# Kernel optimization log

Measured on AMD Instinct MI355X. Metric: run time of the kernel, lower is better.

## Reference

```python
import jax, jax.numpy as jnp
import numpy as np

EPS = 1e-6


def setup_inputs() -> dict:
    key = jax.random.key(0)
    k1, k2, k3 = jax.random.split(key, 3)
    B, S, H, I = 4, 2048, 2048, 8192
    x = jax.random.normal(k1, (B, S, H), dtype=jnp.float32)
    scale = jnp.ones((H,), dtype=jnp.float32)
    ln_bias = jnp.zeros((H,), dtype=jnp.float32)
    # kernel_1: [hidden, num_activations=2, intermediate] (GeGLU)
    kernel_1 = jax.random.normal(k2, (H, 2, I), dtype=jnp.float32) * (1.0 / np.sqrt(H))
    # kernel_2: [intermediate, hidden]
    kernel_2 = jax.random.normal(k3, (I, H), dtype=jnp.float32) * (1.0 / np.sqrt(I))
    return {"x": x, "scale": scale, "ln_bias": ln_bias, "kernel_1": kernel_1, "kernel_2": kernel_2}


def reference(x, scale, ln_bias, kernel_1, kernel_2):
    # LayerNorm over last axis (zero_centered_gamma=False)
    mu = jnp.mean(x, axis=-1, keepdims=True)
    var = jnp.mean(jnp.square(x - mu), axis=-1, keepdims=True)
    y = (x - mu) * jax.lax.rsqrt(var + EPS) * scale + ln_bias
    # First GEMM: [B,S,H] x [H, act=2, I] -> [B,S,2,I]
    h = jnp.einsum("bsh,hai->bsai", y, kernel_1)
    # Gated activation: gelu(branch 0) * linear(branch 1)  (flax gelu: approximate tanh)
    z = jax.nn.gelu(h[..., 0, :], approximate=True) * h[..., 1, :]
    # Dropout rate = 0 (deterministic) -> no-op
    # Second GEMM: [B,S,I] x [I,H] -> [B,S,H]
    out = jnp.einsum("bsi,ih->bsh", z, kernel_2)
    return out
```

## Files before the change

### kernel.cpp

```cpp
#include <hip/hip_runtime.h>
#include <hip/hip_bf16.h>
#include <stdint.h>

typedef __attribute__((ext_vector_type(8))) __bf16 bf16x8;
typedef __attribute__((ext_vector_type(4))) float f32x4;

static constexpr int kTokens = 8192;
static constexpr int kHid    = 2048;
static constexpr int kInter  = 8192;
static constexpr int kN1     = 16384;

__device__ __forceinline__ void async16(const void* g, void* l) {
  using gp = const __attribute__((address_space(1))) unsigned int*;
  using lp = __attribute__((address_space(3))) unsigned int*;
  __builtin_amdgcn_global_load_lds((gp)(uintptr_t)g,
                                   (lp)(unsigned int)(uintptr_t)l, 16, 0, 0);
}

__global__ __launch_bounds__(256) void ln_kernel(
    const float* __restrict__ x, const float* __restrict__ gamma,
    const float* __restrict__ beta, __hip_bfloat16* __restrict__ y) {
  const int t = threadIdx.x;
  const size_t row = blockIdx.x;
  const float* xr = x + row * kHid;
  float4 v0 = ((const float4*)xr)[2 * t];
  float4 v1 = ((const float4*)xr)[2 * t + 1];
  float s  = v0.x + v0.y + v0.z + v0.w + v1.x + v1.y + v1.z + v1.w;
  float s2 = v0.x*v0.x + v0.y*v0.y + v0.z*v0.z + v0.w*v0.w
           + v1.x*v1.x + v1.y*v1.y + v1.z*v1.z + v1.w*v1.w;
#pragma unroll
  for (int off = 1; off < 64; off <<= 1) {
    s  += __shfl_xor(s, off, 64);
    s2 += __shfl_xor(s2, off, 64);
  }
  __shared__ float red[8];
  const int w = t >> 6;
  if ((t & 63) == 0) { red[w] = s; red[4 + w] = s2; }
  __syncthreads();
  s  = red[0] + red[1] + red[2] + red[3];
  s2 = red[4] + red[5] + red[6] + red[7];
  const float mu = s * (1.0f / kHid);
  const float rs = rsqrtf(s2 * (1.0f / kHid) - mu * mu + 1e-6f);
  float4 g0 = ((const float4*)gamma)[2 * t], g1 = ((const float4*)gamma)[2 * t + 1];
  float4 b0 = ((const float4*)beta)[2 * t],  b1 = ((const float4*)beta)[2 * t + 1];
  union { __hip_bfloat16 h[8]; uint4 u; } pk;
  pk.h[0] = __float2bfloat16((v0.x - mu) * rs * g0.x + b0.x);
  pk.h[1] = __float2bfloat16((v0.y - mu) * rs * g0.y + b0.y);
  pk.h[2] = __float2bfloat16((v0.z - mu) * rs * g0.z + b0.z);
  pk.h[3] = __float2bfloat16((v0.w - mu) * rs * g0.w + b0.w);
  pk.h[4] = __float2bfloat16((v1.x - mu) * rs * g1.x + b1.x);
  pk.h[5] = __float2bfloat16((v1.y - mu) * rs * g1.y + b1.y);
  pk.h[6] = __float2bfloat16((v1.z - mu) * rs * g1.z + b1.z);
  pk.h[7] = __float2bfloat16((v1.w - mu) * rs * g1.w + b1.w);
  ((uint4*)(y + row * kHid))[t] = pk.u;
}

template <bool INTERLEAVE>
__global__ __launch_bounds__(256) void cvt_tr(
    const float* __restrict__ src, __hip_bfloat16* __restrict__ dst,
    int K, int N) {
  __shared__ float tile[64][65];
  const int nb = blockIdx.x * 64;
  const int kb = blockIdx.y * 64;
  const int t = threadIdx.x;
#pragma unroll
  for (int it = 0; it < 16; ++it) {
    int p = t + it * 256;
    int lk = p >> 6, ln = p & 63;
    int n = nb + ln;
    int col = INTERLEAVE ? ((((n >> 4) & 1) << 13) + (((n >> 5) << 4) | (n & 15)))
                         : n;
    tile[lk][ln] = src[(size_t)(kb + lk) * N + col];
  }
  __syncthreads();
#pragma unroll
  for (int it = 0; it < 16; ++it) {
    int p = t + it * 256;
    int ln = p >> 6, lk = p & 63;
    dst[(size_t)(nb + ln) * K + kb + lk] = __float2bfloat16(tile[lk][ln]);
  }
}

#define SLOT_A(b, h) ((b) * 65536 + (h) * 16384)
#define SLOT_B(b, h) ((b) * 65536 + 32768 + (h) * 16384)
#define SLOT_DUMMY 131072

template <int EPI, int NXTLOG>
__global__ __launch_bounds__(512, 2) void gemm8p(
    const __hip_bfloat16* __restrict__ A, const __hip_bfloat16* __restrict__ B,
    void* __restrict__ Cout, int M, int N, int K) {
  __shared__ __align__(16) char smem[139264];
  char* const sm = (char*)smem;

  const int t = threadIdx.x;
  const int lane = t & 63;
  const int wave = t >> 6;
  const int wm = wave >> 2;
  const int wn = wave & 3;

  const int nwg = (int)gridDim.x;
  const int wg = ((int)blockIdx.x & 7) * (nwg >> 3) + ((int)blockIdx.x >> 3);
  const int bx = wg & ((1 << NXTLOG) - 1);
  const int by = wg >> NXTLOG;
  const size_t m0 = (size_t)by * 256;
  const size_t n0 = (size_t)bx * 256;

  const int srow = t >> 3;
  const int scsrc = (t & 7) ^ (srow & 7);
  const __hip_bfloat16* const gA = A + (m0 + srow) * K + scsrc * 8;
  const __hip_bfloat16* const gB = B + (n0 + srow) * K + scsrc * 8;
  const size_t K64  = (size_t)64 * K;
  const size_t K128 = (size_t)128 * K;
  const int t16 = t * 16;
  char* const dm = sm + SLOT_DUMMY + t16;

  const int col = lane & 15, q = lane >> 4;
  const int cs0 = (q ^ (col & 7)) * 16;
  const int cs1 = ((4 + q) ^ (col & 7)) * 16;
  const int aO0 = wm * 16384 + col * 128 + cs0;
  const int aO1 = wm * 16384 + col * 128 + cs1;
  const int bO0 = 32768 + (wn >> 1) * 16384 + ((wn & 1) * 64 + col) * 128 + cs0;
  const int bO1 = 32768 + (wn >> 1) * 16384 + ((wn & 1) * 64 + col) * 128 + cs1;

  f32x4 acc[8][4] = {};
  bf16x8 af[4][2], bf[4][2];

  const int NT = K >> 6;
  const int L  = NT >> 1;

#define STG_A(tile, h, buf)                                           \
  do {                                                                \
    const __hip_bfloat16* _s = gA + (size_t)(tile) * 64 + (h) * K128; \
    char* _d = sm + SLOT_A(buf, h) + t16;                             \
    async16(_s, _d);                                                  \
    async16(_s + K64, _d + 8192);                                     \
  } while (0)
#define STG_B(tile, h, buf)                                           \
  do {                                                                \
    const __hip_bfloat16* _s = gB + (size_t)(tile) * 64 + (h) * K128; \
    char* _d = sm + SLOT_B(buf, h) + t16;                             \
    async16(_s, _d);                                                  \
    async16(_s + K64, _d + 8192);                                     \
  } while (0)
#define STG_A_G(tile, h, buf)                  \
  do {                                         \
    if ((tile) < NT) { STG_A(tile, h, buf); }  \
    else { async16(A, dm); async16(A, dm); }   \
  } while (0)
#define STG_B_G(tile, h, buf)                  \
  do {                                         \
    if ((tile) < NT) { STG_B(tile, h, buf); }  \
    else { async16(A, dm); async16(A, dm); }   \
  } while (0)

#define LOAD_A(buf, mh)                                                        \
  { _Pragma("unroll") for (int ii = 0; ii < 4; ++ii) {                         \
      af[ii][0] = *(const bf16x8*)(sm + (buf)*65536 + aO0 + (mh)*8192 + ii*2048); \
      af[ii][1] = *(const bf16x8*)(sm + (buf)*65536 + aO1 + (mh)*8192 + ii*2048); \
  } }
#define LOAD_B(buf, nh)                                                        \
  { _Pragma("unroll") for (int jj = 0; jj < 2; ++jj) {                         \
      bf[(nh)*2 + jj][0] = *(const bf16x8*)(sm + (buf)*65536 + bO0 + ((nh)*2 + jj)*2048); \
      bf[(nh)*2 + jj][1] = *(const bf16x8*)(sm + (buf)*65536 + bO1 + ((nh)*2 + jj)*2048); \
  } }

#define MFMA_QUAD(mh, nh)                                                     \
  { _Pragma("unroll") for (int kk = 0; kk < 2; ++kk)                          \
    _Pragma("unroll") for (int ii = 0; ii < 4; ++ii)                          \
    _Pragma("unroll") for (int jj = 0; jj < 2; ++jj)                          \
      acc[(mh)*4 + ii][(nh)*2 + jj] = __builtin_amdgcn_mfma_f32_16x16x32_bf16( \
          af[ii][kk], bf[(nh)*2 + jj][kk], acc[(mh)*4 + ii][(nh)*2 + jj], 0, 0, 0); }

#define PHASE_MID()                                  \
  __builtin_amdgcn_s_barrier();                      \
  asm volatile("s_waitcnt lgkmcnt(0)" ::: "memory"); \
  __builtin_amdgcn_s_setprio(1)
#define PHASE_MID_VM()                               \
  asm volatile("s_waitcnt vmcnt(4)" ::: "memory");   \
  __builtin_amdgcn_s_barrier();                      \
  asm volatile("s_waitcnt lgkmcnt(0)" ::: "memory"); \
  __builtin_amdgcn_s_setprio(1)
#define PHASE_END()                                  \
  __builtin_amdgcn_s_setprio(0);                     \
  __builtin_amdgcn_s_barrier()

  STG_A(0, 0, 0);
  STG_A(0, 1, 0);
  STG_B(0, 0, 0);
  STG_B(0, 1, 0);
  STG_B(1, 0, 1);
  STG_B(1, 1, 1);
  asm volatile("s_waitcnt vmcnt(4)" ::: "memory");
  __builtin_amdgcn_s_barrier();

#pragma unroll 1
  for (int i = 0; i < L; ++i) {
    const int t1 = 2 * i + 1, t2 = 2 * i + 2, t3 = 2 * i + 3;
    LOAD_A(0, 0) LOAD_B(0, 0)
    STG_A(t1, 0, 1);
    PHASE_MID(); MFMA_QUAD(0, 0) PHASE_END();
    LOAD_B(0, 1)
    STG_A(t1, 1, 1);
    PHASE_MID(); MFMA_QUAD(0, 1) PHASE_END();
    LOAD_A(0, 1)
    STG_B_G(t2, 0, 0);
    PHASE_MID(); MFMA_QUAD(1, 0) PHASE_END();
    STG_B_G(t2, 1, 0);
    PHASE_MID_VM(); MFMA_QUAD(1, 1) PHASE_END();
    LOAD_A(1, 0) LOAD_B(1, 0)
    STG_A_G(t2, 0, 0);
    PHASE_MID(); MFMA_QUAD(0, 0) PHASE_END();
    LOAD_B(1, 1)
    STG_A_G(t2, 1, 0);
    PHASE_MID(); MFMA_QUAD(0, 1) PHASE_END();
    LOAD_A(1, 1)
    STG_B_G(t3, 0, 1);
    PHASE_MID(); MFMA_QUAD(1, 0) PHASE_END();
    STG_B_G(t3, 1, 1);
    PHASE_MID_VM(); MFMA_QUAD(1, 1) PHASE_END();
  }
  asm volatile("s_waitcnt vmcnt(0)" ::: "memory");

  const int gr0 = (int)m0 + wm * 128 + q * 4;
  if (EPI == 0) {
    float* Cf = (float*)Cout;
    const int gc0 = (int)n0 + wn * 64 + col;
#pragma unroll
    for (int mi = 0; mi < 8; ++mi)
#pragma unroll
      for (int j = 0; j < 4; ++j) {
        size_t base = (size_t)(gr0 + mi * 16) * N + gc0 + j * 16;
#pragma unroll
        for (int r = 0; r < 4; ++r) Cf[base + (size_t)r * N] = acc[mi][j][r];
      }
  } else {
    __hip_bfloat16* Z = (__hip_bfloat16*)Cout;
    const int ldz = N >> 1;
    const size_t ib0 = (n0 >> 1) + wn * 32 + col;
#pragma unroll
    for (int mi = 0; mi < 8; ++mi)
#pragma unroll
      for (int tp = 0; tp < 2; ++tp) {
        const f32x4 gg = acc[mi][2 * tp];
        const f32x4 ll = acc[mi][2 * tp + 1];
        size_t base = (size_t)(gr0 + mi * 16) * ldz + ib0 + tp * 16;
#pragma unroll
        for (int r = 0; r < 4; ++r) {
          float xv = gg[r];
          float u = 0.7978845608028654f * xv * (1.0f + 0.044715f * xv * xv);
          float sg = __builtin_amdgcn_rcpf(1.0f + __expf(-2.0f * u));
          Z[base + (size_t)r * ldz] = __float2bfloat16(xv * sg * ll[r]);
        }
      }
  }
}

extern "C" void kernel_launch(void* const* d_in, const int* in_sizes, int n_in,
                              void* d_out, int out_size, void* d_ws, size_t ws_size,
                              hipStream_t stream) {
  const float* x     = (const float*)d_in[0];
  const float* gamma = (const float*)d_in[1];
  const float* beta  = (const float*)d_in[2];
  const float* W1    = (const float*)d_in[3];
  const float* W2    = (const float*)d_in[4];
  float* out = (float*)d_out;

  char* ws = (char*)d_ws;
  __hip_bfloat16* yb  = (__hip_bfloat16*)ws;
  __hip_bfloat16* w1t = (__hip_bfloat16*)(ws + (32ull << 20));
  __hip_bfloat16* w2t = (__hip_bfloat16*)(ws + (96ull << 20));
  __hip_bfloat16* z   = (__hip_bfloat16*)(ws + (128ull << 20));
  (void)in_sizes; (void)n_in; (void)out_size; (void)ws_size;

  ln_kernel<<<kTokens, 256, 0, stream>>>(x, gamma, beta, yb);
  cvt_tr<true ><<<dim3(kN1 / 64, kHid / 64), 256, 0, stream>>>(W1, w1t, kHid, kN1);
  cvt_tr<false><<<dim3(kHid / 64, kInter / 64), 256, 0, stream>>>(W2, w2t, kInter, kHid);
  gemm8p<1, 6><<<dim3((kN1 / 256) * (kTokens / 256)), 512, 0, stream>>>(
      yb, w1t, (void*)z, kTokens, kN1, kHid);
  gemm8p<0, 3><<<dim3((kHid / 256) * (kTokens / 256)), 512, 0, stream>>>(
      z, w2t, (void*)out, kTokens, kHid, kInter);
}
```

Before: 1.003 ms.

## Restructure GEMM prefetch to full-tile double buffering and M-major tile order

The GEMM main loop now stages whole A and B k-tiles (four async loads each) into the alternate buffer two phases ahead, instead of staggering half-tile A loads inside the current iteration. The prologue preloads both buffers, and the wait counts change to vmcnt(8) plus an lgkmcnt(8) wait before the first phase. Workgroup-to-tile mapping also changes from N-fastest to M-fastest (32 M tiles per column), which alters L2 reuse of the weight panels. The deeper prefetch keeps more loads in flight per wave, and the new tile order may reduce reuse of the activation rows.

```diff
diff --git a/kernel.cpp b/kernel.cpp
--- a/kernel.cpp
+++ b/kernel.cpp
@@ -85,7 +85,7 @@
 #define SLOT_B(b, h) ((b) * 65536 + 32768 + (h) * 16384)
 #define SLOT_DUMMY 131072
 
-template <int EPI, int NXTLOG>
+template <int EPI>
 __global__ __launch_bounds__(512, 2) void gemm8p(
     const __hip_bfloat16* __restrict__ A, const __hip_bfloat16* __restrict__ B,
     void* __restrict__ Cout, int M, int N, int K) {
@@ -100,8 +100,8 @@
 
   const int nwg = (int)gridDim.x;
   const int wg = ((int)blockIdx.x & 7) * (nwg >> 3) + ((int)blockIdx.x >> 3);
-  const int bx = wg & ((1 << NXTLOG) - 1);
-  const int by = wg >> NXTLOG;
+  const int by = wg & 31;
+  const int bx = wg >> 5;
   const size_t m0 = (size_t)by * 256;
   const size_t n0 = (size_t)bx * 256;
 
@@ -128,29 +128,35 @@
   const int NT = K >> 6;
   const int L  = NT >> 1;
 
-#define STG_A(tile, h, buf)                                           \
-  do {                                                                \
-    const __hip_bfloat16* _s = gA + (size_t)(tile) * 64 + (h) * K128; \
-    char* _d = sm + SLOT_A(buf, h) + t16;                             \
-    async16(_s, _d);                                                  \
-    async16(_s + K64, _d + 8192);                                     \
-  } while (0)
-#define STG_B(tile, h, buf)                                           \
-  do {                                                                \
-    const __hip_bfloat16* _s = gB + (size_t)(tile) * 64 + (h) * K128; \
-    char* _d = sm + SLOT_B(buf, h) + t16;                             \
-    async16(_s, _d);                                                  \
-    async16(_s + K64, _d + 8192);                                     \
-  } while (0)
-#define STG_A_G(tile, h, buf)                  \
-  do {                                         \
-    if ((tile) < NT) { STG_A(tile, h, buf); }  \
-    else { async16(A, dm); async16(A, dm); }   \
-  } while (0)
-#define STG_B_G(tile, h, buf)                  \
-  do {                                         \
-    if ((tile) < NT) { STG_B(tile, h, buf); }  \
-    else { async16(A, dm); async16(A, dm); }   \
+#define STG_A2(tile, buf)                                \
+  do {                                                   \
+    const __hip_bfloat16* _s = gA + (size_t)(tile) * 64; \
+    char* _d = sm + SLOT_A(buf, 0) + t16;                \
+    async16(_s, _d);                                     \
+    async16(_s + K64, _d + 8192);                        \
+    async16(_s + K128, _d + 16384);                      \
+    async16(_s + K128 + K64, _d + 16384 + 8192);         \
+  } while (0)
+#define STG_B2(tile, buf)                                \
+  do {                                                   \
+    const __hip_bfloat16* _s = gB + (size_t)(tile) * 64; \
+    char* _d = sm + SLOT_B(buf, 0) + t16;                \
+    async16(_s, _d);                                     \
+    async16(_s + K64, _d + 8192);                        \
+    async16(_s + K128, _d + 16384);                      \
+    async16(_s + K128 + K64, _d + 16384 + 8192);         \
+  } while (0)
+#define STG_A2_G(tile, buf)                              \
+  do {                                                   \
+    if ((tile) < NT) { STG_A2(tile, buf); }              \
+    else { async16(A, dm); async16(A, dm);               \
+           async16(A, dm); async16(A, dm); }             \
+  } while (0)
+#define STG_B2_G(tile, buf)                              \
+  do {                                                   \
+    if ((tile) < NT) { STG_B2(tile, buf); }              \
+    else { async16(A, dm); async16(A, dm);               \
+           async16(A, dm); async16(A, dm); }             \
   } while (0)
 
 #define LOAD_A(buf, mh)                                                        \
@@ -175,8 +181,13 @@
   __builtin_amdgcn_s_barrier();                      \
   asm volatile("s_waitcnt lgkmcnt(0)" ::: "memory"); \
   __builtin_amdgcn_s_setprio(1)
+#define PHASE_MID12()                                \
+  asm volatile("s_waitcnt lgkmcnt(8)" ::: "memory"); \
+  __builtin_amdgcn_s_barrier();                      \
+  asm volatile("s_waitcnt lgkmcnt(0)" ::: "memory"); \
+  __builtin_amdgcn_s_setprio(1)
 #define PHASE_MID_VM()                               \
-  asm volatile("s_waitcnt vmcnt(4)" ::: "memory");   \
+  asm volatile("s_waitcnt vmcnt(8)" ::: "memory");   \
   __builtin_amdgcn_s_barrier();                      \
   asm volatile("s_waitcnt lgkmcnt(0)" ::: "memory"); \
   __builtin_amdgcn_s_setprio(1)
@@ -184,39 +195,33 @@
   __builtin_amdgcn_s_setprio(0);                     \
   __builtin_amdgcn_s_barrier()
 
-  STG_A(0, 0, 0);
-  STG_A(0, 1, 0);
-  STG_B(0, 0, 0);
-  STG_B(0, 1, 0);
-  STG_B(1, 0, 1);
-  STG_B(1, 1, 1);
-  asm volatile("s_waitcnt vmcnt(4)" ::: "memory");
+  STG_B2(0, 0);
+  STG_A2(0, 0);
+  STG_B2(1, 1);
+  STG_A2(1, 1);
+  asm volatile("s_waitcnt vmcnt(8)" ::: "memory");
   __builtin_amdgcn_s_barrier();
 
 #pragma unroll 1
   for (int i = 0; i < L; ++i) {
-    const int t1 = 2 * i + 1, t2 = 2 * i + 2, t3 = 2 * i + 3;
+    const int t2 = 2 * i + 2, t3 = 2 * i + 3;
     LOAD_A(0, 0) LOAD_B(0, 0)
-    STG_A(t1, 0, 1);
-    PHASE_MID(); MFMA_QUAD(0, 0) PHASE_END();
+    PHASE_MID12(); MFMA_QUAD(0, 0) PHASE_END();
     LOAD_B(0, 1)
-    STG_A(t1, 1, 1);
     PHASE_MID(); MFMA_QUAD(0, 1) PHASE_END();
     LOAD_A(0, 1)
-    STG_B_G(t2, 0, 0);
+    STG_B2_G(t2, 0);
     PHASE_MID(); MFMA_QUAD(1, 0) PHASE_END();
-    STG_B_G(t2, 1, 0);
+    STG_A2_G(t2, 0);
     PHASE_MID_VM(); MFMA_QUAD(1, 1) PHASE_END();
     LOAD_A(1, 0) LOAD_B(1, 0)
-    STG_A_G(t2, 0, 0);
-    PHASE_MID(); MFMA_QUAD(0, 0) PHASE_END();
+    PHASE_MID12(); MFMA_QUAD(0, 0) PHASE_END();
     LOAD_B(1, 1)
-    STG_A_G(t2, 1, 0);
     PHASE_MID(); MFMA_QUAD(0, 1) PHASE_END();
     LOAD_A(1, 1)
-    STG_B_G(t3, 0, 1);
+    STG_B2_G(t3, 1);
     PHASE_MID(); MFMA_QUAD(1, 0) PHASE_END();
-    STG_B_G(t3, 1, 1);
+    STG_A2_G(t3, 1);
     PHASE_MID_VM(); MFMA_QUAD(1, 1) PHASE_END();
   }
   asm volatile("s_waitcnt vmcnt(0)" ::: "memory");
@@ -275,8 +280,8 @@
   ln_kernel<<<kTokens, 256, 0, stream>>>(x, gamma, beta, yb);
   cvt_tr<true ><<<dim3(kN1 / 64, kHid / 64), 256, 0, stream>>>(W1, w1t, kHid, kN1);
   cvt_tr<false><<<dim3(kHid / 64, kInter / 64), 256, 0, stream>>>(W2, w2t, kInter, kHid);
-  gemm8p<1, 6><<<dim3((kN1 / 256) * (kTokens / 256)), 512, 0, stream>>>(
+  gemm8p<1><<<dim3((kN1 / 256) * (kTokens / 256)), 512, 0, stream>>>(
       yb, w1t, (void*)z, kTokens, kN1, kHid);
-  gemm8p<0, 3><<<dim3((kHid / 256) * (kTokens / 256)), 512, 0, stream>>>(
+  gemm8p<0><<<dim3((kHid / 256) * (kTokens / 256)), 512, 0, stream>>>(
       z, w2t, (void*)out, kTokens, kHid, kInter);
 }
```

Result: slower. 1.053 ms (+5.0%).

## Switch GEMM inner loop to 32x32x16 MFMA with 32-wide gate interleave

Applied to the files above, without the earlier changes.

Replaces the 16x16x32 bf16 MFMA tiling with 32x32x16 MFMA tiles, so each wave holds 4x2 32x32 accumulators. The LDS fragment reads and address precomputation are reworked to fit, and the W1 interleave granularity changes from 16 to 32 columns so gate and linear halves land in matching accumulator tiles. The epilogues are rewritten for the 32x32 output layout. The aim is fewer LDS reads per MFMA and higher MFMA throughput, at the cost of different register pressure and LDS bank-conflict behaviour.

```diff
diff --git a/kernel.cpp b/kernel.cpp
--- a/kernel.cpp
+++ b/kernel.cpp
@@ -4,6 +4,7 @@
 
 typedef __attribute__((ext_vector_type(8))) __bf16 bf16x8;
 typedef __attribute__((ext_vector_type(4))) float f32x4;
+typedef __attribute__((ext_vector_type(16))) float f32x16;
 
 static constexpr int kTokens = 8192;
 static constexpr int kHid    = 2048;
@@ -68,7 +69,7 @@
     int p = t + it * 256;
     int lk = p >> 6, ln = p & 63;
     int n = nb + ln;
-    int col = INTERLEAVE ? ((((n >> 4) & 1) << 13) + (((n >> 5) << 4) | (n & 15)))
+    int col = INTERLEAVE ? ((((n >> 5) & 1) << 13) + (((n >> 6) << 5) | (n & 31)))
                          : n;
     tile[lk][ln] = src[(size_t)(kb + lk) * N + col];
   }
@@ -114,16 +115,20 @@
   const int t16 = t * 16;
   char* const dm = sm + SLOT_DUMMY + t16;
 
-  const int col = lane & 15, q = lane >> 4;
-  const int cs0 = (q ^ (col & 7)) * 16;
-  const int cs1 = ((4 + q) ^ (col & 7)) * 16;
-  const int aO0 = wm * 16384 + col * 128 + cs0;
-  const int aO1 = wm * 16384 + col * 128 + cs1;
-  const int bO0 = 32768 + (wn >> 1) * 16384 + ((wn & 1) * 64 + col) * 128 + cs0;
-  const int bO1 = 32768 + (wn >> 1) * 16384 + ((wn & 1) * 64 + col) * 128 + cs1;
-
-  f32x4 acc[8][4] = {};
-  bf16x8 af[4][2], bf[4][2];
+  const int l31 = lane & 31, hi = lane >> 5, l7 = lane & 7;
+  int aAdr[2][4], bAdr[2][4];
+#pragma unroll
+  for (int b2 = 0; b2 < 2; ++b2)
+#pragma unroll
+    for (int ks = 0; ks < 4; ++ks) {
+      const int ch = (((ks << 1) | hi) ^ l7) << 4;
+      aAdr[b2][ks] = b2 * 65536 + (((wm << 7) + l31) << 7) + ch;
+      bAdr[b2][ks] = b2 * 65536 + 32768 + (((wn << 6) + l31) << 7) + ch;
+    }
+
+  f32x16 acc[4][2] = {};
+  bf16x8 a[2][2];
+  bf16x8 b0[2][2], b1[2][2];
 
   const int NT = K >> 6;
   const int L  = NT >> 1;
@@ -153,23 +158,28 @@
     else { async16(A, dm); async16(A, dm); }   \
   } while (0)
 
-#define LOAD_A(buf, mh)                                                        \
-  { _Pragma("unroll") for (int ii = 0; ii < 4; ++ii) {                         \
-      af[ii][0] = *(const bf16x8*)(sm + (buf)*65536 + aO0 + (mh)*8192 + ii*2048); \
-      af[ii][1] = *(const bf16x8*)(sm + (buf)*65536 + aO1 + (mh)*8192 + ii*2048); \
-  } }
-#define LOAD_B(buf, nh)                                                        \
-  { _Pragma("unroll") for (int jj = 0; jj < 2; ++jj) {                         \
-      bf[(nh)*2 + jj][0] = *(const bf16x8*)(sm + (buf)*65536 + bO0 + ((nh)*2 + jj)*2048); \
-      bf[(nh)*2 + jj][1] = *(const bf16x8*)(sm + (buf)*65536 + bO1 + ((nh)*2 + jj)*2048); \
-  } }
-
-#define MFMA_QUAD(mh, nh)                                                     \
-  { _Pragma("unroll") for (int kk = 0; kk < 2; ++kk)                          \
-    _Pragma("unroll") for (int ii = 0; ii < 4; ++ii)                          \
-    _Pragma("unroll") for (int jj = 0; jj < 2; ++jj)                          \
-      acc[(mh)*4 + ii][(nh)*2 + jj] = __builtin_amdgcn_mfma_f32_16x16x32_bf16( \
-          af[ii][kk], bf[(nh)*2 + jj][kk], acc[(mh)*4 + ii][(nh)*2 + jj], 0, 0, 0); }
+#define RD_A(buf, m, mt, ks, kk) \
+  a[m][kk] = *(const bf16x8*)(sm + aAdr[buf][ks] + (mt) * 4096);
+#define RD_B(buf, dst, nt, ks, kk) \
+  dst[nt][kk] = *(const bf16x8*)(sm + bAdr[buf][ks] + (nt) * 4096);
+
+#define LOAD_A4(buf, mb, kp)            \
+  RD_A(buf, 0, mb,     (kp)*2,     0)   \
+  RD_A(buf, 0, mb,     (kp)*2 + 1, 1)   \
+  RD_A(buf, 1, (mb)+1, (kp)*2,     0)   \
+  RD_A(buf, 1, (mb)+1, (kp)*2 + 1, 1)
+#define LOAD_B4(buf, dst, kp)           \
+  RD_B(buf, dst, 0, (kp)*2,     0)      \
+  RD_B(buf, dst, 0, (kp)*2 + 1, 1)      \
+  RD_B(buf, dst, 1, (kp)*2,     0)      \
+  RD_B(buf, dst, 1, (kp)*2 + 1, 1)
+
+#define MFMA8(mb, Bp)                                                       \
+  { _Pragma("unroll") for (int kk = 0; kk < 2; ++kk)                        \
+    _Pragma("unroll") for (int m = 0; m < 2; ++m)                           \
+    _Pragma("unroll") for (int nt = 0; nt < 2; ++nt)                        \
+      acc[(mb) + m][nt] = __builtin_amdgcn_mfma_f32_32x32x16_bf16(          \
+          a[m][kk], Bp[nt][kk], acc[(mb) + m][nt], 0, 0, 0); }
 
 #define PHASE_MID()                                  \
   __builtin_amdgcn_s_barrier();                      \
@@ -196,62 +206,68 @@
 #pragma unroll 1
   for (int i = 0; i < L; ++i) {
     const int t1 = 2 * i + 1, t2 = 2 * i + 2, t3 = 2 * i + 3;
-    LOAD_A(0, 0) LOAD_B(0, 0)
+    LOAD_A4(0, 0, 0)
+    LOAD_B4(0, b0, 0)
     STG_A(t1, 0, 1);
-    PHASE_MID(); MFMA_QUAD(0, 0) PHASE_END();
-    LOAD_B(0, 1)
+    PHASE_MID(); MFMA8(0, b0) PHASE_END();
+    LOAD_A4(0, 2, 0)
+    LOAD_B4(0, b1, 1)
     STG_A(t1, 1, 1);
-    PHASE_MID(); MFMA_QUAD(0, 1) PHASE_END();
-    LOAD_A(0, 1)
+    PHASE_MID(); MFMA8(2, b0) PHASE_END();
+    LOAD_A4(0, 0, 1)
     STG_B_G(t2, 0, 0);
-    PHASE_MID(); MFMA_QUAD(1, 0) PHASE_END();
+    PHASE_MID(); MFMA8(0, b1) PHASE_END();
+    LOAD_A4(0, 2, 1)
     STG_B_G(t2, 1, 0);
-    PHASE_MID_VM(); MFMA_QUAD(1, 1) PHASE_END();
-    LOAD_A(1, 0) LOAD_B(1, 0)
+    PHASE_MID_VM(); MFMA8(2, b1) PHASE_END();
+    LOAD_A4(1, 0, 0)
+    LOAD_B4(1, b0, 0)
     STG_A_G(t2, 0, 0);
-    PHASE_MID(); MFMA_QUAD(0, 0) PHASE_END();
-    LOAD_B(1, 1)
+    PHASE_MID(); MFMA8(0, b0) PHASE_END();
+    LOAD_A4(1, 2, 0)
+    LOAD_B4(1, b1, 1)
     STG_A_G(t2, 1, 0);
-    PHASE_MID(); MFMA_QUAD(0, 1) PHASE_END();
-    LOAD_A(1, 1)
+    PHASE_MID(); MFMA8(2, b0) PHASE_END();
+    LOAD_A4(1, 0, 1)
     STG_B_G(t3, 0, 1);
-    PHASE_MID(); MFMA_QUAD(1, 0) PHASE_END();
+    PHASE_MID(); MFMA8(0, b1) PHASE_END();
+    LOAD_A4(1, 2, 1)
     STG_B_G(t3, 1, 1);
-    PHASE_MID_VM(); MFMA_QUAD(1, 1) PHASE_END();
+    PHASE_MID_VM(); MFMA8(2, b1) PHASE_END();
   }
   asm volatile("s_waitcnt vmcnt(0)" ::: "memory");
 
-  const int gr0 = (int)m0 + wm * 128 + q * 4;
+  const int gr0 = (int)m0 + wm * 128 + 4 * hi;
   if (EPI == 0) {
     float* Cf = (float*)Cout;
-    const int gc0 = (int)n0 + wn * 64 + col;
-#pragma unroll
-    for (int mi = 0; mi < 8; ++mi)
-#pragma unroll
-      for (int j = 0; j < 4; ++j) {
-        size_t base = (size_t)(gr0 + mi * 16) * N + gc0 + j * 16;
-#pragma unroll
-        for (int r = 0; r < 4; ++r) Cf[base + (size_t)r * N] = acc[mi][j][r];
-      }
+    const int gc0 = (int)n0 + wn * 64 + l31;
+#pragma unroll
+    for (int mt = 0; mt < 4; ++mt)
+#pragma unroll
+      for (int nt = 0; nt < 2; ++nt)
+#pragma unroll
+        for (int g4 = 0; g4 < 4; ++g4)
+#pragma unroll
+          for (int r = 0; r < 4; ++r)
+            Cf[(size_t)(gr0 + mt * 32 + g4 * 8 + r) * N + gc0 + nt * 32] =
+                acc[mt][nt][g4 * 4 + r];
   } else {
     __hip_bfloat16* Z = (__hip_bfloat16*)Cout;
     const int ldz = N >> 1;
-    const size_t ib0 = (n0 >> 1) + wn * 32 + col;
-#pragma unroll
-    for (int mi = 0; mi < 8; ++mi)
-#pragma unroll
-      for (int tp = 0; tp < 2; ++tp) {
-        const f32x4 gg = acc[mi][2 * tp];
-        const f32x4 ll = acc[mi][2 * tp + 1];
-        size_t base = (size_t)(gr0 + mi * 16) * ldz + ib0 + tp * 16;
+    const size_t zc = (n0 >> 1) + wn * 32 + l31;
+#pragma unroll
+    for (int mt = 0; mt < 4; ++mt)
+#pragma unroll
+      for (int g4 = 0; g4 < 4; ++g4)
 #pragma unroll
         for (int r = 0; r < 4; ++r) {
-          float xv = gg[r];
+          const float xv = acc[mt][0][g4 * 4 + r];
+          const float lv = acc[mt][1][g4 * 4 + r];
           float u = 0.7978845608028654f * xv * (1.0f + 0.044715f * xv * xv);
           float sg = __builtin_amdgcn_rcpf(1.0f + __expf(-2.0f * u));
-          Z[base + (size_t)r * ldz] = __float2bfloat16(xv * sg * ll[r]);
+          Z[(size_t)(gr0 + mt * 32 + g4 * 8 + r) * ldz + zc] =
+              __float2bfloat16(xv * sg * lv);
         }
-      }
   }
 }
 
```

New measurement: 1.072 ms. +6.9%, slower.
